# Performance work log

Hardware: AMD Instinct MI355X
Metric: run time of the kernel (lower is better)

Reference implementation:

```python
import jax, jax.numpy as jnp
import numpy as np
from jax import lax

D = 512        # datapathSize (= slow-net hidden size = embedding size)
H = 20         # nonlinearAfterSlowHiddenSize
V = 32000      # softmaxOutputHeadSize = xEmbeddingsNum
T = 1024       # sequence length (number of sequential fast-weight updates)


def setup_inputs() -> dict:
    key = jax.random.key(0)
    ks = jax.random.split(key, 12)
    inp = {}
    inp["tokens"] = jax.random.randint(ks[0], (T,), 0, V)
    inp["targets"] = jax.random.randint(ks[1], (T,), 0, V)
    # learned parameters
    inp["embed"] = jax.random.normal(ks[2], (V, D), dtype=jnp.float32)
    # fastWeightsInit = rand(D,D) * (1/D)
    inp["fw_init"] = jax.random.uniform(ks[3], (D, D), dtype=jnp.float32) * (1.0 / D)
    inp["eta"] = jnp.array(1.0, dtype=jnp.float32)
    inp["wa"] = jax.random.normal(ks[4], (D, D), dtype=jnp.float32) * 0.05
    inp["wb"] = jax.random.normal(ks[5], (D, D), dtype=jnp.float32) * 0.05
    # nonlinearAfterSlow: Linear(D,H) -> selu -> Linear(H,D); stored as (in,out)
    lim_a = 1.0 / np.sqrt(D)
    inp["mlp_aw"] = jax.random.uniform(ks[6], (D, H), dtype=jnp.float32, minval=-lim_a, maxval=lim_a)
    inp["mlp_ab"] = jax.random.uniform(ks[7], (H,), dtype=jnp.float32, minval=-lim_a, maxval=lim_a)
    lim_b = 1.0 / np.sqrt(H)
    inp["mlp_bw"] = jax.random.uniform(ks[8], (H, D), dtype=jnp.float32, minval=-lim_b, maxval=lim_b)
    inp["mlp_bb"] = jax.random.uniform(ks[9], (D,), dtype=jnp.float32, minval=-lim_b, maxval=lim_b)
    # logit head Linear(D, V)
    inp["head_w"] = jax.random.uniform(ks[10], (D, V), dtype=jnp.float32, minval=-lim_a, maxval=lim_a)
    inp["head_b"] = jax.random.uniform(ks[11], (V,), dtype=jnp.float32, minval=-lim_a, maxval=lim_a)
    return inp


def reference(tokens, targets, embed, fw_init, eta, wa, wb,
              mlp_aw, mlp_ab, mlp_bw, mlp_bb, head_w, head_b):
    xs = embed[tokens]  # [T, D]

    def step(fw, x):
        # SlowNetB.forwardAndUpdate for one token
        z0 = x @ wa                      # [D]
        z1 = x @ wb                      # [D]
        fw_new = jnp.tanh(fw + eta * jnp.outer(z0, z1))  # [D, D]
        y = x @ fw_new                   # [D]
        return fw_new, y

    _, ys = lax.scan(step, fw_init, xs)  # ys: [T, D]

    # NonlinearLayer (batched over T)
    h = jax.nn.selu(ys @ mlp_aw + mlp_ab) @ mlp_bw + mlp_bb  # [T, D]
    mixed = 0.5 * h + 0.5 * xs
    logits = mixed @ head_w + head_b     # [T, V]

    logp = jax.nn.log_softmax(logits, axis=-1)
    loss = -jnp.mean(jnp.take_along_axis(logp, targets[:, None], axis=1))
    return logits, loss
```

## Files before the change

### kernel.cpp

```cpp
#include <hip/hip_runtime.h>

#define D 512
#define H 20
#define HP 32
#define V 32000
#define T 1024

typedef unsigned int uint;
typedef __attribute__((ext_vector_type(8))) short short8;
typedef __attribute__((ext_vector_type(4))) float floatx4;

__device__ __forceinline__ unsigned short f2bf(float f) {
    unsigned u = __builtin_bit_cast(unsigned, f);
    u += 0x7fffu + ((u >> 16) & 1u);
    return (unsigned short)(u >> 16);
}

__device__ __forceinline__ float tanh_fast(float x) {
    float t = __builtin_amdgcn_exp2f(x * 2.8853900817779268f);
    float r = __builtin_amdgcn_rcpf(t + 1.0f);
    return __builtin_fmaf(-2.0f, r, 1.0f);
}

template <int CTRL>
__device__ __forceinline__ float dpp_add(float v) {
    int x = __builtin_amdgcn_update_dpp(0, __builtin_bit_cast(int, v), CTRL, 0xf, 0xf, true);
    return v + __builtin_bit_cast(float, x);
}
__device__ __forceinline__ float reduce16(float v) {
    v = dpp_add<0xB1>(v);
    v = dpp_add<0x4E>(v);
    v = dpp_add<0x141>(v);
    v = dpp_add<0x140>(v);
    return v;
}

__global__ __launch_bounds__(256) void gather_kernel(const int* __restrict__ tokens,
                                                     const float* __restrict__ embed,
                                                     float* __restrict__ xs) {
    int idx = blockIdx.x * 256 + threadIdx.x;
    int row = idx >> 7;
    int c   = idx & 127;
    float4 v = ((const float4*)(embed + (long)tokens[row] * D))[c];
    ((float4*)xs)[idx] = v;
}

__global__ __launch_bounds__(256) void zgemm_kernel(const float* __restrict__ xs,
                                                    const float* __restrict__ wa,
                                                    const float* __restrict__ wb,
                                                    float* __restrict__ z0,
                                                    float* __restrict__ z1) {
    __shared__ float Xs[16 * 68];
    __shared__ float Ws[16 * 68];
    const int tid = threadIdx.x;
    const int n0 = blockIdx.x * 64, m0 = blockIdx.y * 64;
    const float* Wm = blockIdx.z ? wb : wa;
    float* Z = blockIdx.z ? z1 : z0;
    const int tx = tid & 15, ty = tid >> 4;
    const int xrow = tid >> 2, xkc = (tid & 3) * 4;
    const int wrow = tid >> 4, wc = (tid & 15) * 4;
    float acc[4][4] = {};
    for (int k0 = 0; k0 < D; k0 += 16) {
        float4 xv = *(const float4*)(xs + (long)(m0 + xrow) * D + k0 + xkc);
        float4 wv = *(const float4*)(Wm + (long)(k0 + wrow) * D + n0 + wc);
        Xs[(xkc + 0) * 68 + xrow] = xv.x;
        Xs[(xkc + 1) * 68 + xrow] = xv.y;
        Xs[(xkc + 2) * 68 + xrow] = xv.z;
        Xs[(xkc + 3) * 68 + xrow] = xv.w;
        *(float4*)(Ws + wrow * 68 + wc) = wv;
        __syncthreads();
#pragma unroll
        for (int k = 0; k < 16; k++) {
            float4 a = *(const float4*)(Xs + k * 68 + ty * 4);
            float4 b = *(const float4*)(Ws + k * 68 + tx * 4);
            float av[4] = {a.x, a.y, a.z, a.w};
            float bv[4] = {b.x, b.y, b.z, b.w};
#pragma unroll
            for (int r = 0; r < 4; r++)
#pragma unroll
                for (int c = 0; c < 4; c++)
                    acc[r][c] = __builtin_fmaf(av[r], bv[c], acc[r][c]);
        }
        __syncthreads();
    }
#pragma unroll
    for (int r = 0; r < 4; r++) {
        float4 v = {acc[r][0], acc[r][1], acc[r][2], acc[r][3]};
        *(float4*)(Z + (long)(m0 + ty * 4 + r) * D + n0 + tx * 4) = v;
    }
}

__global__ __launch_bounds__(256) void scan_kernel(const float* __restrict__ z0,
                                                   const float* __restrict__ z1,
                                                   const float* __restrict__ xs,
                                                   const float* __restrict__ fw_init,
                                                   const float* __restrict__ eta_p,
                                                   float* __restrict__ y) {
    const int tid = threadIdx.x;
    const int j = blockIdx.x;
    const float eta = *eta_p;
    __shared__ float part2[2][8 * 16];
    float f0 = fw_init[(long)tid * D + j];
    float f1 = fw_init[(long)(tid + 256) * D + j];
    float za[8], zb[8], xa[8], xb[8], ez[8];
#pragma unroll
    for (int c = 0; c < 8; c++) {
        const long tr = (long)c * D;
        za[c] = z0[tr + tid];
        zb[c] = z0[tr + tid + 256];
        xa[c] = xs[tr + tid];
        xb[c] = xs[tr + tid + 256];
        ez[c] = z1[tr + j];
    }
    int buf = 0;
    for (int t0 = 0; t0 < T; t0 += 8) {
        float p[8];
#pragma unroll
        for (int c = 0; c < 8; c++) {
            float e = eta * ez[c];
            f0 = tanh_fast(__builtin_fmaf(e, za[c], f0));
            f1 = tanh_fast(__builtin_fmaf(e, zb[c], f1));
            p[c] = xa[c] * f0 + xb[c] * f1;
        }
        if (t0 + 8 < T) {
#pragma unroll
            for (int c = 0; c < 8; c++) {
                const long tr = (long)(t0 + 8 + c) * D;
                za[c] = z0[tr + tid];
                zb[c] = z0[tr + tid + 256];
                xa[c] = xs[tr + tid];
                xb[c] = xs[tr + tid + 256];
                ez[c] = z1[tr + j];
            }
        }
#pragma unroll
        for (int c = 0; c < 8; c++) p[c] = reduce16(p[c]);
        if ((tid & 15) == 0) {
            const int iiH = tid >> 4;
#pragma unroll
            for (int c = 0; c < 8; c++) part2[buf][c * 16 + iiH] = p[c];
        }
        __syncthreads();
        if (tid < 128) {
            const int c = tid >> 4, h = tid & 15;
            float v = part2[buf][c * 16 + h];
            v = reduce16(v);
            if (h == 0) y[(long)(t0 + c) * D + j] = v;
        }
        buf ^= 1;
    }
}

__global__ __launch_bounds__(256) void mlp_a_kernel(const float* __restrict__ y,
                                                    const float* __restrict__ Aw,
                                                    const float* __restrict__ Ab,
                                                    float* __restrict__ hbuf) {
    const int gid = blockIdx.x * 256 + threadIdx.x;
    const int t = gid >> 5, jj = gid & 31;
    if (jj >= H) return;
    float a = 0.f;
    const float* yr = y + (long)t * D;
#pragma unroll 4
    for (int d = 0; d < D; d++) a = __builtin_fmaf(yr[d], Aw[d * H + jj], a);
    a += Ab[jj];
    const float sc = 1.0507009873554805f, al = 1.6732632423543772f;
    hbuf[t * HP + jj] = a > 0.f ? sc * a : sc * al * (__expf(a) - 1.f);
}

__global__ __launch_bounds__(256) void mlp_b_kernel(const float* __restrict__ hbuf,
                                                    const float* __restrict__ xs,
                                                    const float* __restrict__ Bw,
                                                    const float* __restrict__ Bb,
                                                    unsigned short* __restrict__ mixed) {
    const int gid = blockIdx.x * 256 + threadIdx.x;
    const int t = gid >> 9, d = gid & 511;
    float o = Bb[d];
    const float* hr = hbuf + (long)t * HP;
#pragma unroll
    for (int jj = 0; jj < H; jj++) o = __builtin_fmaf(hr[jj], Bw[jj * D + d], o);
    mixed[gid] = f2bf(0.5f * o + 0.5f * xs[gid]);
}

__global__ __launch_bounds__(256) void convert_wt_kernel(const float* __restrict__ head_w,
                                                         unsigned short* __restrict__ wt) {
    __shared__ float tile[64 * 68];
    const int n0 = blockIdx.x * 64, k0 = blockIdx.y * 64;
    const int tid = threadIdx.x;
#pragma unroll
    for (int s = 0; s < 4; s++) {
        int idx4 = s * 256 + tid;
        int r = idx4 >> 4, c4 = idx4 & 15;
        float4 v = *(const float4*)(head_w + (long)(k0 + r) * V + n0 + c4 * 4);
        *(float4*)(tile + r * 68 + c4 * 4) = v;
    }
    __syncthreads();
    const int rr = tid >> 2;
    const int cq = tid & 3;
    uint u[8];
#pragma unroll
    for (int p = 0; p < 8; p++) {
        float a = tile[(cq * 16 + p * 2 + 0) * 68 + rr];
        float b = tile[(cq * 16 + p * 2 + 1) * 68 + rr];
        u[p] = (uint)f2bf(a) | ((uint)f2bf(b) << 16);
    }
    unsigned short* ob = wt + (long)(n0 + rr) * D + k0 + cq * 16;
    uint4 v0 = {u[0], u[1], u[2], u[3]};
    uint4 v1 = {u[4], u[5], u[6], u[7]};
    *(uint4*)ob = v0;
    *((uint4*)ob + 1) = v1;
}

__global__ __launch_bounds__(256) void head_gemm_kernel(const unsigned short* __restrict__ A,
                                                        const unsigned short* __restrict__ Bt,
                                                        const float* __restrict__ bias,
                                                        float* __restrict__ C) {
    __shared__ unsigned short As[128 * 64];
    __shared__ unsigned short Bs[128 * 64];
    const int tid = threadIdx.x;
    const int mt = blockIdx.x & 7, nt = blockIdx.x >> 3;
    const int m0 = mt * 128, n0 = nt * 128;
    const int wave = tid >> 6, lane = tid & 63;
    const int wm = wave >> 1, wn = wave & 1;
    const int quad = lane >> 4, l15 = lane & 15;
    floatx4 acc[4][4] = {};
    for (int k0 = 0; k0 < D; k0 += 64) {
#pragma unroll
        for (int s = 0; s < 4; s++) {
            int idx = s * 256 + tid;
            int row = idx >> 3, slot = idx & 7;
            int gch = slot ^ (row & 7);
            const unsigned short* ga = A + (long)(m0 + row) * D + k0 + gch * 8;
            __builtin_amdgcn_global_load_lds(
                (const __attribute__((address_space(1))) unsigned int*)ga,
                (__attribute__((address_space(3))) unsigned int*)(As + idx * 8), 16, 0, 0);
            const unsigned short* gb = Bt + (long)(n0 + row) * D + k0 + gch * 8;
            __builtin_amdgcn_global_load_lds(
                (const __attribute__((address_space(1))) unsigned int*)gb,
                (__attribute__((address_space(3))) unsigned int*)(Bs + idx * 8), 16, 0, 0);
        }
        __syncthreads();
#pragma unroll
        for (int ks = 0; ks < 2; ks++) {
            short8 af[4], bfr[4];
            int q = ks * 4 + quad;
#pragma unroll
            for (int f = 0; f < 4; f++) {
                int ar = wm * 64 + f * 16 + l15;
                af[f] = *(const short8*)(As + ar * 64 + ((q ^ (ar & 7)) * 8));
                int br = wn * 64 + f * 16 + l15;
                bfr[f] = *(const short8*)(Bs + br * 64 + ((q ^ (br & 7)) * 8));
            }
#pragma unroll
            for (int fr = 0; fr < 4; fr++)
#pragma unroll
                for (int fc = 0; fc < 4; fc++)
                    acc[fr][fc] = __builtin_amdgcn_mfma_f32_16x16x32_bf16(af[fr], bfr[fc],
                                                                          acc[fr][fc], 0, 0, 0);
        }
        __syncthreads();
    }
#pragma unroll
    for (int fc = 0; fc < 4; fc++) {
        int n = n0 + wn * 64 + fc * 16 + l15;
        float b = bias[n];
#pragma unroll
        for (int fr = 0; fr < 4; fr++) {
            int mr = m0 + wm * 64 + fr * 16 + quad * 4;
#pragma unroll
            for (int r = 0; r < 4; r++)
                C[(long)(mr + r) * V + n] = acc[fr][fc][r] + b;
        }
    }
}

__device__ __forceinline__ void lse_upd(float& m, float& s, float v) {
    if (v > m) { s = s * __expf(m - v) + 1.f; m = v; }
    else       { s += __expf(v - m); }
}
__device__ __forceinline__ void lse_comb(float& m, float& s, float m2, float s2) {
    float M = fmaxf(m, m2);
    s = s * __expf(m - M) + s2 * __expf(m2 - M);
    m = M;
}

__global__ __launch_bounds__(256) void loss_rows_kernel(const float* __restrict__ logits,
                                                        const int* __restrict__ targets,
                                                        float* __restrict__ ws_loss) {
    const int t = blockIdx.x, tid = threadIdx.x;
    const float4* row = (const float4*)(logits + (long)t * V);
    float m = -INFINITY, s = 0.f;
    for (int i = tid; i < V / 4; i += 256) {
        float4 v = row[i];
        lse_upd(m, s, v.x); lse_upd(m, s, v.y); lse_upd(m, s, v.z); lse_upd(m, s, v.w);
    }
#pragma unroll
    for (int msk = 1; msk <= 32; msk <<= 1) {
        float m2 = __shfl_xor(m, msk, 64);
        float s2 = __shfl_xor(s, msk, 64);
        lse_comb(m, s, m2, s2);
    }
    __shared__ float sm[4], ss[4];
    if ((tid & 63) == 0) { sm[tid >> 6] = m; ss[tid >> 6] = s; }
    __syncthreads();
    if (tid == 0) {
        float M = sm[0], S = ss[0];
#pragma unroll
        for (int w = 1; w < 4; w++) lse_comb(M, S, sm[w], ss[w]);
        float lse = M + __logf(S);
        float lt = logits[(long)t * V + targets[t]];
        ws_loss[t] = lse - lt;
    }
}

__global__ __launch_bounds__(256) void loss_final_kernel(const float* __restrict__ ws_loss,
                                                         float* __restrict__ out) {
    const int tid = threadIdx.x;
    float s = 0.f;
    for (int i = tid; i < T; i += 256) s += ws_loss[i];
#pragma unroll
    for (int m = 1; m <= 32; m <<= 1) s += __shfl_xor(s, m, 64);
    __shared__ float red[4];
    if ((tid & 63) == 0) red[tid >> 6] = s;
    __syncthreads();
    if (tid == 0) out[0] = (red[0] + red[1] + red[2] + red[3]) * (1.f / (float)T);
}

extern "C" void kernel_launch(void* const* d_in, const int* in_sizes, int n_in,
                              void* d_out, int out_size, void* d_ws, size_t ws_size,
                              hipStream_t stream) {
    const int*   tokens  = (const int*)d_in[0];
    const int*   targets = (const int*)d_in[1];
    const float* embed   = (const float*)d_in[2];
    const float* fw_init = (const float*)d_in[3];
    const float* eta     = (const float*)d_in[4];
    const float* wa      = (const float*)d_in[5];
    const float* wb      = (const float*)d_in[6];
    const float* mlp_aw  = (const float*)d_in[7];
    const float* mlp_ab  = (const float*)d_in[8];
    const float* mlp_bw  = (const float*)d_in[9];
    const float* mlp_bb  = (const float*)d_in[10];
    const float* head_w  = (const float*)d_in[11];
    const float* head_b  = (const float*)d_in[12];
    float* out = (float*)d_out;

    char* ws = (char*)d_ws;
    float*          xs      = (float*)(ws + 0);
    float*          z0      = (float*)(ws + 2097152);
    float*          z1      = (float*)(ws + 4194304);
    float*          y       = (float*)(ws + 6291456);
    unsigned short* mixed   = (unsigned short*)(ws + 8388608);
    unsigned short* wt      = (unsigned short*)(ws + 9437184);
    float*          ws_loss = (float*)(ws + 42205184);
    float*          hbuf    = (float*)(ws + 42209280);

    convert_wt_kernel<<<dim3(V / 64, D / 64), 256, 0, stream>>>(head_w, wt);
    gather_kernel<<<(T * D / 4) / 256, 256, 0, stream>>>(tokens, embed, xs);
    zgemm_kernel<<<dim3(D / 64, T / 64, 2), 256, 0, stream>>>(xs, wa, wb, z0, z1);
    scan_kernel<<<D, 256, 0, stream>>>(z0, z1, xs, fw_init, eta, y);
    mlp_a_kernel<<<(T * HP) / 256, 256, 0, stream>>>(y, mlp_aw, mlp_ab, hbuf);
    mlp_b_kernel<<<(T * D) / 256, 256, 0, stream>>>(hbuf, xs, mlp_bw, mlp_bb, mixed);
    head_gemm_kernel<<<(T / 128) * (V / 128), 256, 0, stream>>>(mixed, wt, head_b, out);
    loss_rows_kernel<<<T, 256, 0, stream>>>(out, targets, ws_loss);
    loss_final_kernel<<<1, 256, 0, stream>>>(ws_loss, out + (long)T * V);
}
```

Baseline: 567.9 us.

## Split scan across single-wave blocks, fuse MLP kernels, shrink zgemm tiles

The sequential scan now runs 2048 single-wavefront blocks, each owning 128 rows of one column. It writes four partial y sums per column, and the MLP kernel adds them up later. This removes the block-wide barrier and shared-memory reduction on every 8-step chunk, and the tanh is reformulated in a pre-scaled domain to save a multiply per step. The two MLP kernels are fused into one per-token kernel that reduces the partials. zgemm uses 32-row tiles to launch more blocks, the workspace is reordered to reuse the z0/z1 region for the bf16 weights, and the weight conversion is moved after the MLP. The cost is extra partial-sum traffic and more blocks resident per column.

```diff
diff --git a/kernel.cpp b/kernel.cpp
--- a/kernel.cpp
+++ b/kernel.cpp
@@ -2,7 +2,6 @@
 
 #define D 512
 #define H 20
-#define HP 32
 #define V 32000
 #define T 1024
 
@@ -14,12 +13,6 @@
     unsigned u = __builtin_bit_cast(unsigned, f);
     u += 0x7fffu + ((u >> 16) & 1u);
     return (unsigned short)(u >> 16);
-}
-
-__device__ __forceinline__ float tanh_fast(float x) {
-    float t = __builtin_amdgcn_exp2f(x * 2.8853900817779268f);
-    float r = __builtin_amdgcn_rcpf(t + 1.0f);
-    return __builtin_fmaf(-2.0f, r, 1.0f);
 }
 
 template <int CTRL>
@@ -50,135 +43,161 @@
                                                     const float* __restrict__ wb,
                                                     float* __restrict__ z0,
                                                     float* __restrict__ z1) {
-    __shared__ float Xs[16 * 68];
+    __shared__ float Xs[16 * 36];
     __shared__ float Ws[16 * 68];
     const int tid = threadIdx.x;
-    const int n0 = blockIdx.x * 64, m0 = blockIdx.y * 64;
+    const int n0 = blockIdx.x * 64, m0 = blockIdx.y * 32;
     const float* Wm = blockIdx.z ? wb : wa;
     float* Z = blockIdx.z ? z1 : z0;
     const int tx = tid & 15, ty = tid >> 4;
-    const int xrow = tid >> 2, xkc = (tid & 3) * 4;
-    const int wrow = tid >> 4, wc = (tid & 15) * 4;
-    float acc[4][4] = {};
+    const int xr = tid >> 3, xk = (tid & 7) * 2;
+    const int wr = tid >> 4, wc = (tid & 15) * 4;
+    float acc[2][4] = {};
     for (int k0 = 0; k0 < D; k0 += 16) {
-        float4 xv = *(const float4*)(xs + (long)(m0 + xrow) * D + k0 + xkc);
-        float4 wv = *(const float4*)(Wm + (long)(k0 + wrow) * D + n0 + wc);
-        Xs[(xkc + 0) * 68 + xrow] = xv.x;
-        Xs[(xkc + 1) * 68 + xrow] = xv.y;
-        Xs[(xkc + 2) * 68 + xrow] = xv.z;
-        Xs[(xkc + 3) * 68 + xrow] = xv.w;
-        *(float4*)(Ws + wrow * 68 + wc) = wv;
+        float2 xv = *(const float2*)(xs + (m0 + xr) * D + k0 + xk);
+        float4 wv = *(const float4*)(Wm + (k0 + wr) * D + n0 + wc);
+        Xs[(xk + 0) * 36 + xr] = xv.x;
+        Xs[(xk + 1) * 36 + xr] = xv.y;
+        *(float4*)(Ws + wr * 68 + wc) = wv;
         __syncthreads();
 #pragma unroll
         for (int k = 0; k < 16; k++) {
-            float4 a = *(const float4*)(Xs + k * 68 + ty * 4);
+            float a0 = Xs[k * 36 + 2 * ty];
+            float a1 = Xs[k * 36 + 2 * ty + 1];
             float4 b = *(const float4*)(Ws + k * 68 + tx * 4);
-            float av[4] = {a.x, a.y, a.z, a.w};
             float bv[4] = {b.x, b.y, b.z, b.w};
 #pragma unroll
-            for (int r = 0; r < 4; r++)
-#pragma unroll
-                for (int c = 0; c < 4; c++)
-                    acc[r][c] = __builtin_fmaf(av[r], bv[c], acc[r][c]);
+            for (int c = 0; c < 4; c++) {
+                acc[0][c] = __builtin_fmaf(a0, bv[c], acc[0][c]);
+                acc[1][c] = __builtin_fmaf(a1, bv[c], acc[1][c]);
+            }
         }
         __syncthreads();
     }
-#pragma unroll
-    for (int r = 0; r < 4; r++) {
-        float4 v = {acc[r][0], acc[r][1], acc[r][2], acc[r][3]};
-        *(float4*)(Z + (long)(m0 + ty * 4 + r) * D + n0 + tx * 4) = v;
-    }
-}
-
-__global__ __launch_bounds__(256) void scan_kernel(const float* __restrict__ z0,
-                                                   const float* __restrict__ z1,
-                                                   const float* __restrict__ xs,
-                                                   const float* __restrict__ fw_init,
-                                                   const float* __restrict__ eta_p,
-                                                   float* __restrict__ y) {
-    const int tid = threadIdx.x;
-    const int j = blockIdx.x;
+    float4 v0 = {acc[0][0], acc[0][1], acc[0][2], acc[0][3]};
+    float4 v1 = {acc[1][0], acc[1][1], acc[1][2], acc[1][3]};
+    *(float4*)(Z + (m0 + 2 * ty + 0) * D + n0 + tx * 4) = v0;
+    *(float4*)(Z + (m0 + 2 * ty + 1) * D + n0 + tx * 4) = v1;
+}
+
+#define CC 2.8853900817779268f
+
+#define LOADC(ZA, ZB, XA, XB, EC, tbase)                       \
+    _Pragma("unroll")                                          \
+    for (int c = 0; c < 8; c++) {                              \
+        int tr = (tbase + c) * D;                              \
+        ZA[c] = z0[tr + i0];                                   \
+        ZB[c] = z0[tr + i1];                                   \
+        XA[c] = xs[tr + i0];                                   \
+        XB[c] = xs[tr + i1];                                   \
+        EC[c] = z1[tr + j] * ETAC;                             \
+    }
+
+#define COMPUTE(ZA, ZB, XA, XB, EC, tbase)                     \
+    {                                                          \
+        float p[8];                                            \
+        _Pragma("unroll")                                      \
+        for (int c = 0; c < 8; c++) {                          \
+            float e = EC[c];                                   \
+            float e0 = __builtin_amdgcn_exp2f(__builtin_fmaf(e, ZA[c], g0)); \
+            float e1 = __builtin_amdgcn_exp2f(__builtin_fmaf(e, ZB[c], g1)); \
+            float r0 = __builtin_amdgcn_rcpf(e0 + 1.0f);       \
+            float r1 = __builtin_amdgcn_rcpf(e1 + 1.0f);       \
+            g0 = __builtin_fmaf(-2.0f * CC, r0, CC);           \
+            g1 = __builtin_fmaf(-2.0f * CC, r1, CC);           \
+            p[c] = XA[c] * g0 + XB[c] * g1;                    \
+        }                                                      \
+        _Pragma("unroll")                                      \
+        for (int c = 0; c < 8; c++) {                          \
+            float v = reduce16(p[c]);                          \
+            v += __shfl_xor(v, 16, 64);                        \
+            v += __shfl_xor(v, 32, 64);                        \
+            p[c] = v;                                          \
+        }                                                      \
+        if (lane == 0) {                                       \
+            _Pragma("unroll")                                  \
+            for (int c = 0; c < 8; c++) yp[(tbase + c) * D] = p[c]; \
+        }                                                      \
+    }
+
+__global__ __launch_bounds__(64) void scan_kernel(const float* __restrict__ z0,
+                                                  const float* __restrict__ z1,
+                                                  const float* __restrict__ xs,
+                                                  const float* __restrict__ fw_init,
+                                                  const float* __restrict__ eta_p,
+                                                  float* __restrict__ ypart) {
+    const int lane = threadIdx.x;
+    const int bid = blockIdx.x;
+    const int j = bid & 511;
+    const int q = bid >> 9;
+    const int i0 = q * 128 + lane;
+    const int i1 = i0 + 64;
     const float eta = *eta_p;
-    __shared__ float part2[2][8 * 16];
-    float f0 = fw_init[(long)tid * D + j];
-    float f1 = fw_init[(long)(tid + 256) * D + j];
-    float za[8], zb[8], xa[8], xb[8], ez[8];
-#pragma unroll
-    for (int c = 0; c < 8; c++) {
-        const long tr = (long)c * D;
-        za[c] = z0[tr + tid];
-        zb[c] = z0[tr + tid + 256];
-        xa[c] = xs[tr + tid];
-        xb[c] = xs[tr + tid + 256];
-        ez[c] = z1[tr + j];
-    }
-    int buf = 0;
-    for (int t0 = 0; t0 < T; t0 += 8) {
-        float p[8];
-#pragma unroll
-        for (int c = 0; c < 8; c++) {
-            float e = eta * ez[c];
-            f0 = tanh_fast(__builtin_fmaf(e, za[c], f0));
-            f1 = tanh_fast(__builtin_fmaf(e, zb[c], f1));
-            p[c] = xa[c] * f0 + xb[c] * f1;
-        }
-        if (t0 + 8 < T) {
-#pragma unroll
-            for (int c = 0; c < 8; c++) {
-                const long tr = (long)(t0 + 8 + c) * D;
-                za[c] = z0[tr + tid];
-                zb[c] = z0[tr + tid + 256];
-                xa[c] = xs[tr + tid];
-                xb[c] = xs[tr + tid + 256];
-                ez[c] = z1[tr + j];
-            }
-        }
-#pragma unroll
-        for (int c = 0; c < 8; c++) p[c] = reduce16(p[c]);
-        if ((tid & 15) == 0) {
-            const int iiH = tid >> 4;
-#pragma unroll
-            for (int c = 0; c < 8; c++) part2[buf][c * 16 + iiH] = p[c];
-        }
-        __syncthreads();
-        if (tid < 128) {
-            const int c = tid >> 4, h = tid & 15;
-            float v = part2[buf][c * 16 + h];
-            v = reduce16(v);
-            if (h == 0) y[(long)(t0 + c) * D + j] = v;
-        }
-        buf ^= 1;
-    }
-}
-
-__global__ __launch_bounds__(256) void mlp_a_kernel(const float* __restrict__ y,
-                                                    const float* __restrict__ Aw,
-                                                    const float* __restrict__ Ab,
-                                                    float* __restrict__ hbuf) {
-    const int gid = blockIdx.x * 256 + threadIdx.x;
-    const int t = gid >> 5, jj = gid & 31;
-    if (jj >= H) return;
-    float a = 0.f;
-    const float* yr = y + (long)t * D;
-#pragma unroll 4
-    for (int d = 0; d < D; d++) a = __builtin_fmaf(yr[d], Aw[d * H + jj], a);
-    a += Ab[jj];
-    const float sc = 1.0507009873554805f, al = 1.6732632423543772f;
-    hbuf[t * HP + jj] = a > 0.f ? sc * a : sc * al * (__expf(a) - 1.f);
-}
-
-__global__ __launch_bounds__(256) void mlp_b_kernel(const float* __restrict__ hbuf,
-                                                    const float* __restrict__ xs,
-                                                    const float* __restrict__ Bw,
-                                                    const float* __restrict__ Bb,
-                                                    unsigned short* __restrict__ mixed) {
-    const int gid = blockIdx.x * 256 + threadIdx.x;
-    const int t = gid >> 9, d = gid & 511;
-    float o = Bb[d];
-    const float* hr = hbuf + (long)t * HP;
-#pragma unroll
-    for (int jj = 0; jj < H; jj++) o = __builtin_fmaf(hr[jj], Bw[jj * D + d], o);
-    mixed[gid] = f2bf(0.5f * o + 0.5f * xs[gid]);
+    const float ETAC = eta * CC;
+    float g0 = CC * fw_init[(long)i0 * D + j];
+    float g1 = CC * fw_init[(long)i1 * D + j];
+    float* yp = ypart + (long)q * T * D + j;
+
+    float zaA[8], zbA[8], xaA[8], xbA[8], ecA[8];
+    float zaB[8], zbB[8], xaB[8], xbB[8], ecB[8];
+    LOADC(zaA, zbA, xaA, xbA, ecA, 0);
+    for (int t0 = 0; t0 < T; t0 += 16) {
+        LOADC(zaB, zbB, xaB, xbB, ecB, t0 + 8);
+        COMPUTE(zaA, zbA, xaA, xbA, ecA, t0);
+        if (t0 + 16 < T) { LOADC(zaA, zbA, xaA, xbA, ecA, t0 + 16); }
+        COMPUTE(zaB, zbB, xaB, xbB, ecB, t0 + 8);
+    }
+}
+
+__global__ __launch_bounds__(256) void mlp_fused_kernel(const float* __restrict__ ypart,
+                                                        const float* __restrict__ xs,
+                                                        const float* __restrict__ Aw,
+                                                        const float* __restrict__ Ab,
+                                                        const float* __restrict__ Bw,
+                                                        const float* __restrict__ Bb,
+                                                        unsigned short* __restrict__ mixed) {
+    const int t = blockIdx.x, tid = threadIdx.x;
+    __shared__ float y_lds[D];
+    __shared__ float h_lds[H];
+    const float INVC = 0.34657359027997264f;
+#pragma unroll
+    for (int s = 0; s < 2; s++) {
+        int d = s * 256 + tid;
+        float v = ypart[(0 * T + t) * D + d] + ypart[(1 * T + t) * D + d]
+                + ypart[(2 * T + t) * D + d] + ypart[(3 * T + t) * D + d];
+        y_lds[d] = v * INVC;
+    }
+    __syncthreads();
+    const int w = tid >> 6, lane = tid & 63;
+    float yv[8];
+#pragma unroll
+    for (int k = 0; k < 8; k++) yv[k] = y_lds[k * 64 + lane];
+#pragma unroll
+    for (int u = 0; u < 5; u++) {
+        const int jj = w * 5 + u;
+        float a = 0.f;
+#pragma unroll
+        for (int k = 0; k < 8; k++)
+            a = __builtin_fmaf(yv[k], Aw[(k * 64 + lane) * H + jj], a);
+        a = reduce16(a);
+        a += __shfl_xor(a, 16, 64);
+        a += __shfl_xor(a, 32, 64);
+        if (lane == 0) {
+            a += Ab[jj];
+            const float sc = 1.0507009873554805f, al = 1.6732632423543772f;
+            h_lds[jj] = a > 0.f ? sc * a : sc * al * (__expf(a) - 1.f);
+        }
+    }
+    __syncthreads();
+#pragma unroll
+    for (int s = 0; s < 2; s++) {
+        int d = s * 256 + tid;
+        float o = Bb[d];
+#pragma unroll
+        for (int jj = 0; jj < H; jj++) o = __builtin_fmaf(h_lds[jj], Bw[jj * D + d], o);
+        int gi = t * D + d;
+        mixed[gi] = f2bf(0.5f * o + 0.5f * xs[gi]);
+    }
 }
 
 __global__ __launch_bounds__(256) void convert_wt_kernel(const float* __restrict__ head_w,
@@ -347,18 +366,16 @@
     float*          xs      = (float*)(ws + 0);
     float*          z0      = (float*)(ws + 2097152);
     float*          z1      = (float*)(ws + 4194304);
-    float*          y       = (float*)(ws + 6291456);
-    unsigned short* mixed   = (unsigned short*)(ws + 8388608);
-    unsigned short* wt      = (unsigned short*)(ws + 9437184);
-    float*          ws_loss = (float*)(ws + 42205184);
-    float*          hbuf    = (float*)(ws + 42209280);
-
+    float*          ypart   = (float*)(ws + 6291456);
+    unsigned short* wt      = (unsigned short*)(ws + 2097152);
+    unsigned short* mixed   = (unsigned short*)(ws + 35651584);
+    float*          ws_loss = (float*)(ws + 36700160);
+
+    gather_kernel<<<(T * D / 4) / 256, 256, 0, stream>>>(tokens, embed, xs);
+    zgemm_kernel<<<dim3(D / 64, T / 32, 2), 256, 0, stream>>>(xs, wa, wb, z0, z1);
+    scan_kernel<<<2048, 64, 0, stream>>>(z0, z1, xs, fw_init, eta, ypart);
+    mlp_fused_kernel<<<T, 256, 0, stream>>>(ypart, xs, mlp_aw, mlp_ab, mlp_bw, mlp_bb, mixed);
     convert_wt_kernel<<<dim3(V / 64, D / 64), 256, 0, stream>>>(head_w, wt);
-    gather_kernel<<<(T * D / 4) / 256, 256, 0, stream>>>(tokens, embed, xs);
-    zgemm_kernel<<<dim3(D / 64, T / 64, 2), 256, 0, stream>>>(xs, wa, wb, z0, z1);
-    scan_kernel<<<D, 256, 0, stream>>>(z0, z1, xs, fw_init, eta, y);
-    mlp_a_kernel<<<(T * HP) / 256, 256, 0, stream>>>(y, mlp_aw, mlp_ab, hbuf);
-    mlp_b_kernel<<<(T * D) / 256, 256, 0, stream>>>(hbuf, xs, mlp_bw, mlp_bb, mixed);
     head_gemm_kernel<<<(T / 128) * (V / 128), 256, 0, stream>>>(mixed, wt, head_b, out);
     loss_rows_kernel<<<T, 256, 0, stream>>>(out, targets, ws_loss);
     loss_final_kernel<<<1, 256, 0, stream>>>(ws_loss, out + (long)T * V);
```

Result: faster. 521.1 us (-8.3%).
